# Optimization experiments

Hardware: AMD Instinct MI355X
Metric: run time of the kernel (lower is better)

The kernel has to match this reference:

```python
import jax, jax.numpy as jnp
import numpy as np

B, L, T, IN, H, OUT = 1024, 64, 128, 13, 64, 13
NEG = -1e30


def gru_step(x, h, Wih, Whh, bih, bhh):
    # PyTorch GRU cell: gates ordered (r, z, n)
    gi = x @ Wih.T + bih          # [B, 3H]
    gh = h @ Whh.T + bhh          # [B, 3H]
    ir, iz, inn = jnp.split(gi, 3, axis=-1)
    hr, hz, hn = jnp.split(gh, 3, axis=-1)
    r = jax.nn.sigmoid(ir + hr)
    z = jax.nn.sigmoid(iz + hz)
    n = jnp.tanh(inn + r * hn)
    return (1.0 - z) * n + z * h


def setup_inputs() -> dict:
    key = jax.random.key(0)
    ks = jax.random.split(key, 10)
    s = float(1.0 / np.sqrt(H))
    x = jax.random.normal(ks[0], (B, L, IN), jnp.float32)
    lengths = jax.random.randint(ks[1], (B,), 1, L + 1).at[0].set(L)
    Wih = jax.random.uniform(ks[2], (3 * H, IN), jnp.float32, -s, s)
    Whh = jax.random.uniform(ks[3], (3 * H, H), jnp.float32, -s, s)
    bih = jax.random.uniform(ks[4], (3 * H,), jnp.float32, -s, s)
    bhh = jax.random.uniform(ks[5], (3 * H,), jnp.float32, -s, s)
    Wf = jax.random.uniform(ks[6], (OUT, H), jnp.float32, -s, s)
    bf = jax.random.uniform(ks[7], (OUT,), jnp.float32, -s, s)
    Wa = jax.random.uniform(ks[8], (H, H), jnp.float32, -s, s)
    ba = jax.random.uniform(ks[9], (H,), jnp.float32, -s, s)
    return dict(x=x, lengths=lengths, output_length=T, Wih=Wih, Whh=Whh,
                bih=bih, bhh=bhh, Wf=Wf, bf=bf, Wa=Wa, ba=ba)


def reference(x, lengths, output_length, Wih, Whh, bih, bhh, Wf, bf, Wa, ba):
    b, l = x.shape[0], x.shape[1]
    xT = jnp.swapaxes(x, 0, 1)                        # [L, B, IN]
    h0 = jnp.zeros((b, H), x.dtype)

    # Encoder: masked GRU emulating pack_padded/pad_packed semantics:
    # hidden frozen past each sequence's length; outputs zero past length.
    def enc(h, inp):
        t, xt = inp
        hn = gru_step(xt, h, Wih, Whh, bih, bhh)
        valid = (t < lengths)[:, None]
        h = jnp.where(valid, hn, h)
        return h, jnp.where(valid, hn, 0.0)

    h, outs = jax.lax.scan(enc, h0, (jnp.arange(l), xT))
    # output[:, -1, :] of the padded output (zeros for seqs shorter than max)
    nin = outs[-1] @ Wf.T + bf                        # [B, OUT]

    Tn = output_length
    buf0 = jnp.zeros((Tn, b, H), x.dtype)             # growing past-prediction buffer

    def dec(carry, t):
        h, buf, nin = carry
        hn = gru_step(nin, h, Wih, Whh, bih, bhh)     # output_lstm == hidden (1 layer, 1 step)
        # attention recomputed over all past predictions (softmax over time axis)
        logits = jnp.einsum('tbh,gh->tbg', buf, Wa) + ba      # [T, B, H]
        logits = jnp.where((jnp.arange(Tn) < t)[:, None, None], logits, NEG)
        w = jax.nn.softmax(logits, axis=0)
        o = hn + jnp.sum(w * buf, axis=0)             # at t=0 buffer is all zeros -> +0
        y = o @ Wf.T + bf
        return (hn, buf.at[t].set(o), y), y

    _, ys = jax.lax.scan(dec, (h, buf0, nin), jnp.arange(Tn))
    return jnp.swapaxes(ys, 0, 1)                     # [B, T, OUT]
```

## Files before the change

### kernel.cpp

```cpp
#include <hip/hip_runtime.h>
#include <stdint.h>
#include <math.h>

#define BATCH 1024
#define SEQL  64
#define TDEC  128
#define NIN   13
#define NH    64
#define NOUT  13

typedef _Float16 h2 __attribute__((ext_vector_type(2)));
typedef __fp16   g2 __attribute__((ext_vector_type(2)));

union FU  { uint32_t u; float f; };
union HU  { uint16_t u; _Float16 h; };
union H2U { uint32_t u; h2 h; g2 g; };

__device__ __forceinline__ float bf2f(uint16_t v) { FU t; t.u = ((uint32_t)v) << 16; return t.f; }
__device__ __forceinline__ float hf2f(uint16_t v) { HU t; t.u = v; return (float)t.h; }

__device__ __forceinline__ float ldf(const void* p, long i, int mode) {
    if (mode == 1) return bf2f(((const uint16_t*)p)[i]);
    if (mode == 2) return hf2f(((const uint16_t*)p)[i]);
    return ((const float*)p)[i];
}

__device__ __forceinline__ bool pass_stats(const void* p, int n, int lane, int mode,
                                           float band_lo, float band_hi, float max_ok) {
    int m = (n + 1) / 2;
    int cnt = (m < 64) ? m : 64;
    bool ok_max = true, in_band = false;
    if (lane < cnt) {
        long pos = 2L * (((long)lane * m) / cnt);
        float v = (mode == 1) ? bf2f(((const uint16_t*)p)[pos])
                              : hf2f(((const uint16_t*)p)[pos]);
        float a = fabsf(v);
        ok_max  = (a <= max_ok);
        in_band = (a >= band_lo && a <= band_hi);
    }
    bool allmax = __all(ok_max);
    int nb = (int)__popcll(__ballot(in_band));
    int need = cnt / 4; if (need < 1) need = 1;
    return allmax && (nb >= need);
}
__device__ __forceinline__ int detect(const void* p, int n, int lane,
                                      float band_lo, float band_hi, float max_ok) {
    if (pass_stats(p, n, lane, 1, band_lo, band_hi, max_ok)) return 1;
    if (pass_stats(p, n, lane, 2, band_lo, band_hi, max_ok)) return 2;
    return 0;
}
__device__ __forceinline__ bool detect_len64(const int* p, int lane) {
    int v = p[2 * lane + 1];
    return __all(v == 0);
}

__device__ __forceinline__ float dot2(h2 a, h2 b, float c) {
#if __has_builtin(__builtin_amdgcn_fdot2)
    return __builtin_amdgcn_fdot2(a, b, c, false);
#else
    return c + (float)a[0] * (float)b[0] + (float)a[1] * (float)b[1];
#endif
}
__device__ __forceinline__ uint32_t pku(float a, float b) {
    H2U t; t.g = __builtin_amdgcn_cvt_pkrtz(a, b); return t.u;
}
__device__ __forceinline__ h2 uh(uint32_t u) { H2U t; t.u = u; return t.h; }
__device__ __forceinline__ float rcp_(float x) { return __builtin_amdgcn_rcpf(x); }
__device__ __forceinline__ float exp2_(float x) {
#if __has_builtin(__builtin_amdgcn_exp2f)
    return __builtin_amdgcn_exp2f(x);
#else
    return __expf(x * 0.69314718056f);
#endif
}
__device__ __forceinline__ float sigm2(float xs)  { return rcp_(1.0f + exp2_(-xs)); }
__device__ __forceinline__ float tanh2(float xs)  { return 1.0f - 2.0f * rcp_(exp2_(xs) + 1.0f); }

__device__ __forceinline__ float swap1(float v) {
    FU a; a.f = v;
    FU b; b.u = (uint32_t)__builtin_amdgcn_mov_dpp((int)a.u, 0xB1, 0xF, 0xF, true);
    return b.f;
}

#define BCAST32(vreg, dst)                                                 \
    {                                                                      \
        uint32_t _pr = pku((vreg), swap1(vreg));                           \
        _Pragma("unroll")                                                  \
        for (int _k = 0; _k < 32; ++_k)                                    \
            (dst)[_k] = __builtin_amdgcn_readlane(_pr, 2 * _k);            \
    }

#define DEC_STEP(T_, YSLOT)                                                        \
    {                                                                              \
        float arA = bcr, azA = bcz, hnA = bnh, anA = bni;                          \
        float arB = 0.0f, azB = 0.0f, hnB = 0.0f;                                  \
        float arC = 0.0f, azC = 0.0f, hnC = 0.0f;                                  \
        float arD = 0.0f, azD = 0.0f, hnD = 0.0f;                                  \
        _Pragma("unroll")                                                          \
        for (int k = 0; k < 32; k += 4) {                                          \
            h2 h0 = uh(hpk[k]), h1 = uh(hpk[k + 1]);                               \
            h2 h2v = uh(hpk[k + 2]), h3 = uh(hpk[k + 3]);                          \
            arA = dot2(whhr[k],     h0, arA); azA = dot2(whhz[k],     h0, azA); hnA = dot2(whhn[k],     h0, hnA); \
            arB = dot2(whhr[k + 1], h1, arB); azB = dot2(whhz[k + 1], h1, azB); hnB = dot2(whhn[k + 1], h1, hnB); \
            arC = dot2(whhr[k + 2], h2v, arC); azC = dot2(whhz[k + 2], h2v, azC); hnC = dot2(whhn[k + 2], h2v, hnC); \
            arD = dot2(whhr[k + 3], h3, arD); azD = dot2(whhz[k + 3], h3, azD); hnD = dot2(whhn[k + 3], h3, hnD); \
        }                                                                          \
        _Pragma("unroll")                                                          \
        for (int p = 0; p < 7; ++p) {                                              \
            h2 xv = uh(ypk[p]);                                                    \
            arB = dot2(wihr[p], xv, arB);                                          \
            azB = dot2(wihz[p], xv, azB);                                          \
            anA = dot2(wihn[p], xv, anA);                                          \
        }                                                                          \
        float ar = (arA + arB) + (arC + arD);                                      \
        float az = (azA + azB) + (azC + azD);                                      \
        float hna = (hnA + hnB) + (hnC + hnD);                                     \
        float r_ = sigm2(ar);                                                      \
        float z_ = sigm2(az);                                                      \
        float n_ = tanh2(anA + r_ * hna);                                          \
        float hnew = n_ + z_ * (h - n_);                                           \
        h = hnew;                                                                  \
        float attn = ((T_) > 0) ? num * rcp_(Zs) : 0.0f;                           \
        float o_ = hnew + attn;                                                    \
        BCAST32(hnew, hpk);                                                        \
        uint32_t opk[32];                                                          \
        BCAST32(o_, opk);                                                          \
        float sA = baj, yA = bfj, sB = 0.0f, yB = 0.0f;                            \
        float sC = 0.0f, yC = 0.0f, sD = 0.0f, yD = 0.0f;                          \
        _Pragma("unroll")                                                          \
        for (int k = 0; k < 32; k += 4) {                                          \
            h2 o0 = uh(opk[k]), o1 = uh(opk[k + 1]);                               \
            h2 o2 = uh(opk[k + 2]), o3 = uh(opk[k + 3]);                           \
            sA = dot2(wap[k],     o0, sA); yA = dot2(wfp[k],     o0, yA);          \
            sB = dot2(wap[k + 1], o1, sB); yB = dot2(wfp[k + 1], o1, yB);          \
            sC = dot2(wap[k + 2], o2, sC); yC = dot2(wfp[k + 2], o2, yC);          \
            sD = dot2(wap[k + 3], o3, sD); yD = dot2(wfp[k + 3], o3, yD);          \
        }                                                                          \
        float s_  = (sA + sB) + (sC + sD);                                         \
        float yv_ = (yA + yB) + (yC + yD);                                         \
        float mn = fmaxf(m, s_);                                                   \
        float al = exp2_(m - mn);                                                  \
        float pp = exp2_(s_ - mn);                                                 \
        Zs  = Zs * al + pp;                                                        \
        num = num * al + pp * o_;                                                  \
        m = mn;                                                                    \
        YSLOT = yv_;                                                               \
        float yz = (j < NOUT) ? yv_ : 0.0f;                                        \
        uint32_t pr_ = pku(yz, swap1(yz));                                         \
        _Pragma("unroll")                                                          \
        for (int k = 0; k < 7; ++k) ypk[k] = __builtin_amdgcn_readlane(pr_, 2 * k);\
    }

__global__ __launch_bounds__(64, 1)
void gru_attn_kernel(const void* __restrict__ x, const int* __restrict__ lengths,
                     const void* __restrict__ Wih, const void* __restrict__ Whh,
                     const void* __restrict__ bih, const void* __restrict__ bhh,
                     const void* __restrict__ Wf, const void* __restrict__ bfv,
                     const void* __restrict__ Wa, const void* __restrict__ ba,
                     float* __restrict__ out)
{
    const int b = blockIdx.x;
    const int j = threadIdx.x;

    const int dX   = detect(x,   BATCH * SEQL * NIN, j, 0.25f, 4.0f, 16.0f);
    const int dWih = detect(Wih, 3 * NH * NIN, j, 0.04f, 0.13f, 0.14f);
    const int dWhh = detect(Whh, 3 * NH * NH,  j, 0.04f, 0.13f, 0.14f);
    const int dBih = detect(bih, 3 * NH,       j, 0.04f, 0.13f, 0.14f);
    const int dBhh = detect(bhh, 3 * NH,       j, 0.04f, 0.13f, 0.14f);
    const int dWf  = detect(Wf,  NOUT * NH,    j, 0.04f, 0.13f, 0.14f);
    const int dBf  = detect(bfv, NOUT,         j, 0.04f, 0.13f, 0.14f);
    const int dWa  = detect(Wa,  NH * NH,      j, 0.04f, 0.13f, 0.14f);
    const int dBa  = detect(ba,  NH,           j, 0.04f, 0.13f, 0.14f);
    const bool len64 = detect_len64(lengths, j);

    const float L2E  = 1.44269504089f;
    const float L2E2 = 2.88539008177f;

    h2 wihr[7], wihz[7], wihn[7];
    h2 whhr[32], whhz[32], whhn[32];
    h2 wap[32], wfp[32];

#pragma unroll
    for (int k = 0; k < 7; ++k) {
        float a0 = ldf(Wih, (0 * NH + j) * NIN + 2 * k, dWih);
        float a1 = (2 * k + 1 < NIN) ? ldf(Wih, (0 * NH + j) * NIN + 2 * k + 1, dWih) : 0.0f;
        wihr[k] = uh(pku(a0 * L2E, a1 * L2E));
        float b0 = ldf(Wih, (1 * NH + j) * NIN + 2 * k, dWih);
        float b1 = (2 * k + 1 < NIN) ? ldf(Wih, (1 * NH + j) * NIN + 2 * k + 1, dWih) : 0.0f;
        wihz[k] = uh(pku(b0 * L2E, b1 * L2E));
        float c0 = ldf(Wih, (2 * NH + j) * NIN + 2 * k, dWih);
        float c1 = (2 * k + 1 < NIN) ? ldf(Wih, (2 * NH + j) * NIN + 2 * k + 1, dWih) : 0.0f;
        wihn[k] = uh(pku(c0 * L2E2, c1 * L2E2));
    }
    const int jf = (j < NOUT) ? j : 0;
#pragma unroll
    for (int k = 0; k < 32; ++k) {
        whhr[k] = uh(pku(ldf(Whh, (0 * NH + j) * NH + 2 * k, dWhh) * L2E,
                         ldf(Whh, (0 * NH + j) * NH + 2 * k + 1, dWhh) * L2E));
        whhz[k] = uh(pku(ldf(Whh, (1 * NH + j) * NH + 2 * k, dWhh) * L2E,
                         ldf(Whh, (1 * NH + j) * NH + 2 * k + 1, dWhh) * L2E));
        whhn[k] = uh(pku(ldf(Whh, (2 * NH + j) * NH + 2 * k, dWhh) * L2E2,
                         ldf(Whh, (2 * NH + j) * NH + 2 * k + 1, dWhh) * L2E2));
        wap[k]  = uh(pku(ldf(Wa, j * NH + 2 * k, dWa) * L2E,
                         ldf(Wa, j * NH + 2 * k + 1, dWa) * L2E));
        wfp[k]  = uh(pku(ldf(Wf, jf * NH + 2 * k, dWf),
                         ldf(Wf, jf * NH + 2 * k + 1, dWf)));
    }

    const float bcr = (ldf(bih, j, dBih)      + ldf(bhh, j, dBhh))      * L2E;
    const float bcz = (ldf(bih, NH + j, dBih) + ldf(bhh, NH + j, dBhh)) * L2E;
    const float bni = ldf(bih, 2 * NH + j, dBih) * L2E2;
    const float bnh = ldf(bhh, 2 * NH + j, dBhh) * L2E2;
    const float baj = ldf(ba, j, dBa) * L2E;
    const float bfj = ldf(bfv, jf, dBf);
    const int len = len64 ? lengths[2 * b] : lengths[b];

    uint32_t xp[7];
    {
        const long base = ((long)b * SEQL + j) * NIN;
        float v[14];
#pragma unroll
        for (int k = 0; k < NIN; ++k) v[k] = ldf(x, base + k, dX);
        v[13] = 0.0f;
#pragma unroll
        for (int p = 0; p < 7; ++p) xp[p] = pku(v[2 * p], v[2 * p + 1]);
    }

    float h = 0.0f;
    float out_last = 0.0f;

    uint32_t hpk[32];
#pragma unroll
    for (int k = 0; k < 32; ++k) hpk[k] = 0u;

#pragma unroll 2
    for (int t = 0; t < SEQL; ++t) {
        uint32_t xw[7];
#pragma unroll
        for (int p = 0; p < 7; ++p) xw[p] = __builtin_amdgcn_readlane(xp[p], t);

        float arA = bcr, azA = bcz, hnA = bnh, anA = bni;
        float arB = 0.0f, azB = 0.0f, hnB = 0.0f;
        float arC = 0.0f, azC = 0.0f, hnC = 0.0f;
        float arD = 0.0f, azD = 0.0f, hnD = 0.0f;
#pragma unroll
        for (int k = 0; k < 32; k += 4) {
            h2 h0 = uh(hpk[k]), h1 = uh(hpk[k + 1]), h2v = uh(hpk[k + 2]), h3 = uh(hpk[k + 3]);
            arA = dot2(whhr[k],     h0, arA); azA = dot2(whhz[k],     h0, azA); hnA = dot2(whhn[k],     h0, hnA);
            arB = dot2(whhr[k + 1], h1, arB); azB = dot2(whhz[k + 1], h1, azB); hnB = dot2(whhn[k + 1], h1, hnB);
            arC = dot2(whhr[k + 2], h2v, arC); azC = dot2(whhz[k + 2], h2v, azC); hnC = dot2(whhn[k + 2], h2v, hnC);
            arD = dot2(whhr[k + 3], h3, arD); azD = dot2(whhz[k + 3], h3, azD); hnD = dot2(whhn[k + 3], h3, hnD);
        }
#pragma unroll
        for (int p = 0; p < 7; ++p) {
            h2 xv = uh(xw[p]);
            arB = dot2(wihr[p], xv, arB);
            azB = dot2(wihz[p], xv, azB);
            anA = dot2(wihn[p], xv, anA);
        }
        float ar = (arA + arB) + (arC + arD);
        float az = (azA + azB) + (azC + azD);
        float hna = (hnA + hnB) + (hnC + hnD);
        float r = sigm2(ar);
        float z = sigm2(az);
        float n = tanh2(anA + r * hna);
        float hnew = n + z * (h - n);
        bool upd = (t < len);
        h = upd ? hnew : h;
        if (t == SEQL - 1) out_last = upd ? hnew : 0.0f;
        BCAST32(h, hpk);
    }

    uint32_t ypk[7];
    {
        uint32_t opk[32];
        BCAST32(out_last, opk);
        float nA = bfj, nB = 0.0f, nC = 0.0f, nD = 0.0f;
#pragma unroll
        for (int k = 0; k < 32; k += 4) {
            nA = dot2(wfp[k],     uh(opk[k]),     nA);
            nB = dot2(wfp[k + 1], uh(opk[k + 1]), nB);
            nC = dot2(wfp[k + 2], uh(opk[k + 2]), nC);
            nD = dot2(wfp[k + 3], uh(opk[k + 3]), nD);
        }
        float nv = (nA + nB) + (nC + nD);
        float nz = (j < NOUT) ? nv : 0.0f;
        uint32_t pr = pku(nz, swap1(nz));
#pragma unroll
        for (int k = 0; k < 7; ++k) ypk[k] = __builtin_amdgcn_readlane(pr, 2 * k);
    }

    float m = -1e30f, Zs = 0.0f, num = 0.0f;

#pragma unroll 1
    for (int t0 = 0; t0 < TDEC; t0 += 4) {
        float y0, y1, y2, y3;
        DEC_STEP(t0 + 0, y0);
        DEC_STEP(t0 + 1, y1);
        DEC_STEP(t0 + 2, y2);
        DEC_STEP(t0 + 3, y3);
        if (j < NOUT) {
            size_t base_ = ((size_t)b * TDEC + t0) * NOUT + j;
            out[base_]            = y0;
            out[base_ + NOUT]     = y1;
            out[base_ + 2 * NOUT] = y2;
            out[base_ + 3 * NOUT] = y3;
        }
    }
}

extern "C" void kernel_launch(void* const* d_in, const int* in_sizes, int n_in,
                              void* d_out, int out_size, void* d_ws, size_t ws_size,
                              hipStream_t stream) {
    (void)in_sizes; (void)n_in; (void)out_size; (void)d_ws; (void)ws_size;
    const void* x      = d_in[0];
    const int* lengths = (const int*)d_in[1];
    const void* Wih = d_in[3];
    const void* Whh = d_in[4];
    const void* bih = d_in[5];
    const void* bhh = d_in[6];
    const void* Wf  = d_in[7];
    const void* bf  = d_in[8];
    const void* Wa  = d_in[9];
    const void* ba  = d_in[10];
    float* out = (float*)d_out;

    gru_attn_kernel<<<dim3(BATCH), dim3(64), 0, stream>>>(
        x, lengths, Wih, Whh, bih, bhh, Wf, bf, Wa, ba, out);
}
```

Baseline: 228.9 us.

## Broadcast hidden state through LDS ping-pong buffers instead of readlane chains

Replaces the 32-readlane broadcast of the packed hidden and output vectors with one packed LDS write per even lane plus four 128-bit LDS reads per lane, using double-buffered shared arrays so each step reads one buffer and writes the other. Encoder inputs are also staged in LDS instead of read back with per-step readlanes, and the decoder's y feedback broadcast is moved ahead of the softmax update. This removes the long serial scalar readlane chains from the recurrence's critical path. In exchange it adds LDS latency and depends on wave-level ordering (a single 64-lane wave with only wave barriers), which may be fragile.

```diff
diff --git a/kernel.cpp b/kernel.cpp
--- a/kernel.cpp
+++ b/kernel.cpp
@@ -75,6 +75,7 @@
 }
 __device__ __forceinline__ float sigm2(float xs)  { return rcp_(1.0f + exp2_(-xs)); }
 __device__ __forceinline__ float tanh2(float xs)  { return 1.0f - 2.0f * rcp_(exp2_(xs) + 1.0f); }
+__device__ __forceinline__ void wb() { __builtin_amdgcn_wave_barrier(); }
 
 __device__ __forceinline__ float swap1(float v) {
     FU a; a.f = v;
@@ -82,16 +83,28 @@
     return b.f;
 }
 
-#define BCAST32(vreg, dst)                                                 \
+#define BWRITE(DSTB, V)                                                    \
     {                                                                      \
-        uint32_t _pr = pku((vreg), swap1(vreg));                           \
+        float _w  = swap1(V);                                              \
+        float _lo = odd ? _w  : (V);                                       \
+        float _hi = odd ? (V) : _w;                                        \
+        (DSTB)[jhalf] = pku(_lo, _hi);                                     \
+    }
+
+#define BREAD(SRC, DST)                                                    \
+    {                                                                      \
         _Pragma("unroll")                                                  \
-        for (int _k = 0; _k < 32; ++_k)                                    \
-            (dst)[_k] = __builtin_amdgcn_readlane(_pr, 2 * _k);            \
-    }
-
-#define DEC_STEP(T_, YSLOT)                                                        \
+        for (int _k = 0; _k < 32; _k += 4) {                               \
+            uint4 _q = *(const uint4*)((SRC) + _k);                        \
+            (DST)[_k]     = _q.x; (DST)[_k + 1] = _q.y;                    \
+            (DST)[_k + 2] = _q.z; (DST)[_k + 3] = _q.w;                    \
+        }                                                                  \
+    }
+
+#define DEC_STEP(T_, HRD, HWR, OB_, YSLOT)                                         \
     {                                                                              \
+        uint32_t hpk[32];                                                          \
+        BREAD(HRD, hpk);                                                           \
         float arA = bcr, azA = bcz, hnA = bnh, anA = bni;                          \
         float arB = 0.0f, azB = 0.0f, hnB = 0.0f;                                  \
         float arC = 0.0f, azC = 0.0f, hnC = 0.0f;                                  \
@@ -120,11 +133,12 @@
         float n_ = tanh2(anA + r_ * hna);                                          \
         float hnew = n_ + z_ * (h - n_);                                           \
         h = hnew;                                                                  \
+        BWRITE(HWR, hnew);                                                         \
         float attn = ((T_) > 0) ? num * rcp_(Zs) : 0.0f;                           \
         float o_ = hnew + attn;                                                    \
-        BCAST32(hnew, hpk);                                                        \
+        BWRITE(OB_, o_);                                                           \
         uint32_t opk[32];                                                          \
-        BCAST32(o_, opk);                                                          \
+        BREAD(OB_, opk);                                                           \
         float sA = baj, yA = bfj, sB = 0.0f, yB = 0.0f;                            \
         float sC = 0.0f, yC = 0.0f, sD = 0.0f, yD = 0.0f;                          \
         _Pragma("unroll")                                                          \
@@ -136,19 +150,61 @@
             sC = dot2(wap[k + 2], o2, sC); yC = dot2(wfp[k + 2], o2, yC);          \
             sD = dot2(wap[k + 3], o3, sD); yD = dot2(wfp[k + 3], o3, yD);          \
         }                                                                          \
+        float yv_ = (yA + yB) + (yC + yD);                                         \
+        YSLOT = yv_;                                                               \
+        float yz = (j < NOUT) ? yv_ : 0.0f;                                        \
+        uint32_t pr_ = pku(yz, swap1(yz));                                         \
+        _Pragma("unroll")                                                          \
+        for (int k = 0; k < 7; ++k) ypk[k] = __builtin_amdgcn_readlane(pr_, 2 * k);\
         float s_  = (sA + sB) + (sC + sD);                                         \
-        float yv_ = (yA + yB) + (yC + yD);                                         \
         float mn = fmaxf(m, s_);                                                   \
         float al = exp2_(m - mn);                                                  \
         float pp = exp2_(s_ - mn);                                                 \
         Zs  = Zs * al + pp;                                                        \
         num = num * al + pp * o_;                                                  \
         m = mn;                                                                    \
-        YSLOT = yv_;                                                               \
-        float yz = (j < NOUT) ? yv_ : 0.0f;                                        \
-        uint32_t pr_ = pku(yz, swap1(yz));                                         \
-        _Pragma("unroll")                                                          \
-        for (int k = 0; k < 7; ++k) ypk[k] = __builtin_amdgcn_readlane(pr_, 2 * k);\
+    }
+
+#define ENC_STEP(T_, HRD, HWR)                                                     \
+    {                                                                              \
+        uint32_t hpk[32];                                                          \
+        BREAD(HRD, hpk);                                                           \
+        uint4 q0 = *(const uint4*)(&xs2[(T_)][0]);                                 \
+        uint4 q1 = *(const uint4*)(&xs2[(T_)][4]);                                 \
+        float arA = bcr, azA = bcz, hnA = bnh, anA = bni;                          \
+        float arB = 0.0f, azB = 0.0f, hnB = 0.0f;                                  \
+        float arC = 0.0f, azC = 0.0f, hnC = 0.0f;                                  \
+        float arD = 0.0f, azD = 0.0f, hnD = 0.0f;                                  \
+        _Pragma("unroll")                                                          \
+        for (int k = 0; k < 32; k += 4) {                                          \
+            h2 h0 = uh(hpk[k]), h1 = uh(hpk[k + 1]);                               \
+            h2 h2v = uh(hpk[k + 2]), h3 = uh(hpk[k + 3]);                          \
+            arA = dot2(whhr[k],     h0, arA); azA = dot2(whhz[k],     h0, azA); hnA = dot2(whhn[k],     h0, hnA); \
+            arB = dot2(whhr[k + 1], h1, arB); azB = dot2(whhz[k + 1], h1, azB); hnB = dot2(whhn[k + 1], h1, hnB); \
+            arC = dot2(whhr[k + 2], h2v, arC); azC = dot2(whhz[k + 2], h2v, azC); hnC = dot2(whhn[k + 2], h2v, hnC); \
+            arD = dot2(whhr[k + 3], h3, arD); azD = dot2(whhz[k + 3], h3, azD); hnD = dot2(whhn[k + 3], h3, hnD); \
+        }                                                                          \
+        {                                                                          \
+            uint32_t xw[8] = {q0.x, q0.y, q0.z, q0.w, q1.x, q1.y, q1.z, q1.w};     \
+            _Pragma("unroll")                                                      \
+            for (int p = 0; p < 7; ++p) {                                          \
+                h2 xv = uh(xw[p]);                                                 \
+                arB = dot2(wihr[p], xv, arB);                                      \
+                azB = dot2(wihz[p], xv, azB);                                      \
+                anA = dot2(wihn[p], xv, anA);                                      \
+            }                                                                      \
+        }                                                                          \
+        float ar = (arA + arB) + (arC + arD);                                      \
+        float az = (azA + azB) + (azC + azD);                                      \
+        float hna = (hnA + hnB) + (hnC + hnD);                                     \
+        float r_ = sigm2(ar);                                                      \
+        float z_ = sigm2(az);                                                      \
+        float n_ = tanh2(anA + r_ * hna);                                          \
+        float hnew = n_ + z_ * (h - n_);                                           \
+        bool upd = ((T_) < len);                                                   \
+        h = upd ? hnew : h;                                                        \
+        if ((T_) == SEQL - 1) out_last = upd ? hnew : 0.0f;                        \
+        BWRITE(HWR, h);                                                            \
     }
 
 __global__ __launch_bounds__(64, 1)
@@ -161,6 +217,12 @@
 {
     const int b = blockIdx.x;
     const int j = threadIdx.x;
+    const bool odd = j & 1;
+    const int jhalf = j >> 1;
+
+    __shared__ __align__(16) uint32_t xs2[SEQL][8];
+    __shared__ __align__(16) uint32_t hb[2][32];
+    __shared__ __align__(16) uint32_t ob[2][32];
 
     const int dX   = detect(x,   BATCH * SEQL * NIN, j, 0.25f, 4.0f, 16.0f);
     const int dWih = detect(Wih, 3 * NH * NIN, j, 0.04f, 0.13f, 0.14f);
@@ -215,7 +277,6 @@
     const float bfj = ldf(bfv, jf, dBf);
     const int len = len64 ? lengths[2 * b] : lengths[b];
 
-    uint32_t xp[7];
     {
         const long base = ((long)b * SEQL + j) * NIN;
         float v[14];
@@ -223,58 +284,27 @@
         for (int k = 0; k < NIN; ++k) v[k] = ldf(x, base + k, dX);
         v[13] = 0.0f;
 #pragma unroll
-        for (int p = 0; p < 7; ++p) xp[p] = pku(v[2 * p], v[2 * p + 1]);
-    }
+        for (int p = 0; p < 7; ++p) xs2[j][p] = pku(v[2 * p], v[2 * p + 1]);
+        xs2[j][7] = 0u;
+    }
+    wb();
 
     float h = 0.0f;
     float out_last = 0.0f;
 
-    uint32_t hpk[32];
-#pragma unroll
-    for (int k = 0; k < 32; ++k) hpk[k] = 0u;
-
-#pragma unroll 2
-    for (int t = 0; t < SEQL; ++t) {
-        uint32_t xw[7];
-#pragma unroll
-        for (int p = 0; p < 7; ++p) xw[p] = __builtin_amdgcn_readlane(xp[p], t);
-
-        float arA = bcr, azA = bcz, hnA = bnh, anA = bni;
-        float arB = 0.0f, azB = 0.0f, hnB = 0.0f;
-        float arC = 0.0f, azC = 0.0f, hnC = 0.0f;
-        float arD = 0.0f, azD = 0.0f, hnD = 0.0f;
-#pragma unroll
-        for (int k = 0; k < 32; k += 4) {
-            h2 h0 = uh(hpk[k]), h1 = uh(hpk[k + 1]), h2v = uh(hpk[k + 2]), h3 = uh(hpk[k + 3]);
-            arA = dot2(whhr[k],     h0, arA); azA = dot2(whhz[k],     h0, azA); hnA = dot2(whhn[k],     h0, hnA);
-            arB = dot2(whhr[k + 1], h1, arB); azB = dot2(whhz[k + 1], h1, azB); hnB = dot2(whhn[k + 1], h1, hnB);
-            arC = dot2(whhr[k + 2], h2v, arC); azC = dot2(whhz[k + 2], h2v, azC); hnC = dot2(whhn[k + 2], h2v, hnC);
-            arD = dot2(whhr[k + 3], h3, arD); azD = dot2(whhz[k + 3], h3, azD); hnD = dot2(whhn[k + 3], h3, hnD);
-        }
-#pragma unroll
-        for (int p = 0; p < 7; ++p) {
-            h2 xv = uh(xw[p]);
-            arB = dot2(wihr[p], xv, arB);
-            azB = dot2(wihz[p], xv, azB);
-            anA = dot2(wihn[p], xv, anA);
-        }
-        float ar = (arA + arB) + (arC + arD);
-        float az = (azA + azB) + (azC + azD);
-        float hna = (hnA + hnB) + (hnC + hnD);
-        float r = sigm2(ar);
-        float z = sigm2(az);
-        float n = tanh2(anA + r * hna);
-        float hnew = n + z * (h - n);
-        bool upd = (t < len);
-        h = upd ? hnew : h;
-        if (t == SEQL - 1) out_last = upd ? hnew : 0.0f;
-        BCAST32(h, hpk);
+    BWRITE(&hb[0][0], 0.0f);
+
+#pragma unroll 1
+    for (int t0 = 0; t0 < SEQL; t0 += 2) {
+        ENC_STEP(t0,     (&hb[0][0]), (&hb[1][0]));
+        ENC_STEP(t0 + 1, (&hb[1][0]), (&hb[0][0]));
     }
 
     uint32_t ypk[7];
     {
+        BWRITE(&ob[0][0], out_last);
         uint32_t opk[32];
-        BCAST32(out_last, opk);
+        BREAD(&ob[0][0], opk);
         float nA = bfj, nB = 0.0f, nC = 0.0f, nD = 0.0f;
 #pragma unroll
         for (int k = 0; k < 32; k += 4) {
@@ -295,10 +325,10 @@
 #pragma unroll 1
     for (int t0 = 0; t0 < TDEC; t0 += 4) {
         float y0, y1, y2, y3;
-        DEC_STEP(t0 + 0, y0);
-        DEC_STEP(t0 + 1, y1);
-        DEC_STEP(t0 + 2, y2);
-        DEC_STEP(t0 + 3, y3);
+        DEC_STEP(t0 + 0, (&hb[0][0]), (&hb[1][0]), (&ob[0][0]), y0);
+        DEC_STEP(t0 + 1, (&hb[1][0]), (&hb[0][0]), (&ob[1][0]), y1);
+        DEC_STEP(t0 + 2, (&hb[0][0]), (&hb[1][0]), (&ob[0][0]), y2);
+        DEC_STEP(t0 + 3, (&hb[1][0]), (&hb[0][0]), (&ob[1][0]), y3);
         if (j < NOUT) {
             size_t base_ = ((size_t)b * TDEC + t0) * NOUT + j;
             out[base_]            = y0;
```

After: 210.3 us. -8.1%, faster.
